# Performance work log

Measured on AMD Instinct MI355X. Metric: run time of the kernel, lower is better.

Reference implementation:

```python
import jax, jax.numpy as jnp
import numpy as np

NOPE, ROPE, LORA, VDIM = 128, 64, 512, 128
H, T = 16, 2048
SCALE = 1.0 / float(np.sqrt(NOPE + ROPE))  # 192**-0.5


def setup_inputs() -> dict:
    key = jax.random.key(0)
    k1, k2, k3, k4, k5 = jax.random.split(key, 5)
    return {
        "query": jax.random.normal(k1, (T, H, NOPE + ROPE), jnp.float32),
        "k_c_normed": jax.random.normal(k2, (T, LORA), jnp.float32),
        "k_pe": jax.random.normal(k3, (T, ROPE), jnp.float32),
        "w_kv_b": jax.random.normal(k4, (LORA, H * (NOPE + VDIM)), jnp.float32) * 0.02,
        "w_uv": jax.random.normal(k5, (H, LORA, VDIM), jnp.float32) * 0.02,
    }


def reference(query, k_c_normed, k_pe, w_kv_b, w_uv):
    # Causal (fresh-token, "compute friendly") MLA path of HPUUnifiedMLAImpl.
    t = query.shape[0]
    # kv_b_proj: latent -> per-head [nope | v]; only k_nope is used for scoring
    kv_nope = (k_c_normed @ w_kv_b).reshape(t, H, NOPE + VDIM)
    k_nope = kv_nope[..., :NOPE]                                   # [T,H,128]
    # k = cat(k_nope, broadcast k_pe) -> [T,H,192]
    k = jnp.concatenate(
        [k_nope, jnp.broadcast_to(k_pe[:, None, :], (t, H, ROPE))], axis=-1)
    # causal attention scores [H,T,T]
    scores = jnp.einsum('thd,shd->hts', query, k) * SCALE
    mask = jnp.tril(jnp.ones((t, t), dtype=bool))                  # causal
    scores = jnp.where(mask[None], scores, jnp.finfo(scores.dtype).min)
    p = jax.nn.softmax(scores, axis=-1)
    # value is the latent k_c, shared across heads (v_causal_latent expand)
    out_latent = jnp.einsum('hts,sl->thl', p, k_c_normed)          # [T,H,512]
    # W_UV projects latent attn output -> full v dim
    out = jnp.einsum('thl,hlv->thv', out_latent, w_uv)             # [T,H,128]
    return out.reshape(t, H * VDIM)
```

## Files before the change

### kernel.cpp

```cpp
#include <hip/hip_runtime.h>
#include <hip/hip_bf16.h>
#include <math.h>

#define T_SEQ 2048
#define NHEAD 16
#define DQK 192
#define DNOPE 128
#define DROPE 64
#define LORA_D 512
#define VDIM 128
#define SCALE_F 0.072168783648703216f
#define KC 32

typedef short bf16x8 __attribute__((ext_vector_type(8)));
typedef float f32x4 __attribute__((ext_vector_type(4)));

static __device__ __forceinline__ unsigned short f2bf(float x) {
  union { float f; unsigned int u; } v; v.f = x;
  unsigned int r = (v.u + 0x7fff + ((v.u >> 16) & 1)) >> 16;
  return (unsigned short)r;
}

__global__ __launch_bounds__(256) void stage_all(
    const float* __restrict__ k_c, const float* __restrict__ w_kv_b,
    const float* __restrict__ w_uv, unsigned short* __restrict__ Ab,
    unsigned short* __restrict__ BkT, unsigned short* __restrict__ BvT)
{
  __shared__ float tile[32][33];
  const int bx = blockIdx.x, role = blockIdx.y;
  const int tid = threadIdx.x;
  if (role == 0) {
    int i = (bx * 256 + tid) * 4;
    float4 v = *(const float4*)(k_c + i);
    ushort4 o = {f2bf(v.x), f2bf(v.y), f2bf(v.z), f2bf(v.w)};
    *(ushort4*)(Ab + i) = o;
    return;
  }
  const int tk = tid >> 3, tc4 = (tid & 7) * 4;
  const int wr = tid >> 3, wk4 = (tid & 7) * 4;
  if (role == 1) {
    const int k0 = (bx & 15) * 32, n0 = (bx >> 4) * 32;
    int n = n0 + tc4;
    int col = n + ((n >> 7) << 7);
    float4 v = *(const float4*)&w_kv_b[(size_t)(k0 + tk) * 4096 + col];
    tile[tk][tc4 + 0] = v.x; tile[tk][tc4 + 1] = v.y;
    tile[tk][tc4 + 2] = v.z; tile[tk][tc4 + 3] = v.w;
    __syncthreads();
    ushort4 o = {f2bf(tile[wk4 + 0][wr]), f2bf(tile[wk4 + 1][wr]),
                 f2bf(tile[wk4 + 2][wr]), f2bf(tile[wk4 + 3][wr])};
    *(ushort4*)&BkT[(size_t)(n0 + wr) * LORA_D + k0 + wk4] = o;
  } else {
    const int k0 = (bx & 15) * 32, v0 = ((bx >> 4) & 3) * 32, h = bx >> 6;
    float4 v = *(const float4*)&w_uv[(size_t)h * 65536 + (size_t)(k0 + tk) * 128 + v0 + tc4];
    tile[tk][tc4 + 0] = v.x; tile[tk][tc4 + 1] = v.y;
    tile[tk][tc4 + 2] = v.z; tile[tk][tc4 + 3] = v.w;
    __syncthreads();
    ushort4 o = {f2bf(tile[wk4 + 0][wr]), f2bf(tile[wk4 + 1][wr]),
                 f2bf(tile[wk4 + 2][wr]), f2bf(tile[wk4 + 3][wr])};
    *(ushort4*)&BvT[(size_t)(h * VDIM + v0 + wr) * LORA_D + k0 + wk4] = o;
  }
}

__global__ __launch_bounds__(256) void prep_gemm(
    const unsigned short* __restrict__ A, const unsigned short* __restrict__ BkT,
    const unsigned short* __restrict__ BvT, const float* __restrict__ k_pe,
    unsigned short* __restrict__ Kb, unsigned short* __restrict__ Vt)
{
  __shared__ unsigned short SMEM[32768];
  const int m0 = blockIdx.x * 128;
  const int by = blockIdx.y;
  const int isK = (by < 16);
  const int n0 = (isK ? by : (by - 16)) * 128;
  const unsigned short* BT = isK ? BkT : BvT;
  const int tid = threadIdx.x;
  const int wid = tid >> 6, lane = tid & 63;
  const int l16 = lane & 15, quad = lane >> 4;
  const int wm = (wid >> 1) * 64, wn = (wid & 1) * 64;

  auto stage_pg = [&](int b, int k0) {
    const char* Asrc = (const char*)(A + (size_t)m0 * LORA_D + k0);
    const char* Bsrc = (const char*)(BT + (size_t)n0 * LORA_D + k0);
    char* Adst = (char*)SMEM + b * 16384;
    char* Bdst = (char*)SMEM + 32768 + b * 16384;
#pragma unroll
    for (int i = 0; i < 4; ++i) {
      int d = tid * 16 + i * 4096;
      int row = d >> 7, c = d & 127;
      int sc = c ^ ((row & 7) << 4);
      __builtin_amdgcn_global_load_lds(
          (const unsigned int*)(Asrc + (size_t)row * 1024 + sc),
          (unsigned int*)(Adst + d), 16, 0, 0);
      __builtin_amdgcn_global_load_lds(
          (const unsigned int*)(Bsrc + (size_t)row * 1024 + sc),
          (unsigned int*)(Bdst + d), 16, 0, 0);
    }
  };

  f32x4 acc[4][4];
#pragma unroll
  for (int i = 0; i < 4; ++i)
#pragma unroll
    for (int j = 0; j < 4; ++j) acc[i][j] = (f32x4){0.f, 0.f, 0.f, 0.f};

  stage_pg(0, 0);
  __syncthreads();
  for (int kc = 0; kc < 8; ++kc) {
    const int cur = kc & 1;
    if (kc < 7) stage_pg(cur ^ 1, (kc + 1) * 64);
#pragma unroll
    for (int kk = 0; kk < 2; ++kk) {
      bf16x8 af[4], bfr[4];
#pragma unroll
      for (int t = 0; t < 4; ++t) {
        int ra = wm + t * 16 + l16;
        af[t] = *(const bf16x8*)((char*)SMEM + cur * 16384 + ra * 128 +
                                 (((kk * 4 + quad) ^ (ra & 7)) << 4));
        int rb = wn + t * 16 + l16;
        bfr[t] = *(const bf16x8*)((char*)SMEM + 32768 + cur * 16384 + rb * 128 +
                                  (((kk * 4 + quad) ^ (rb & 7)) << 4));
      }
#pragma unroll
      for (int mt = 0; mt < 4; ++mt)
#pragma unroll
        for (int nt = 0; nt < 4; ++nt)
          acc[mt][nt] = __builtin_amdgcn_mfma_f32_16x16x32_bf16(af[mt], bfr[nt], acc[mt][nt], 0, 0, 0);
    }
    __syncthreads();
  }

  unsigned short* E = SMEM;
  if (isK) {
#pragma unroll
    for (int mt = 0; mt < 4; ++mt)
#pragma unroll
      for (int nt = 0; nt < 4; ++nt) {
        int ml = wm + mt * 16 + quad * 4;
        int d = wn + nt * 16 + l16;
#pragma unroll
        for (int r = 0; r < 4; ++r)
          E[(ml + r) * 136 + d] = f2bf(acc[mt][nt][r]);
      }
  } else {
#pragma unroll
    for (int mt = 0; mt < 4; ++mt)
#pragma unroll
      for (int nt = 0; nt < 4; ++nt) {
        int ml = wm + mt * 16 + quad * 4;
        int nl = wn + nt * 16 + l16;
#pragma unroll
        for (int r = 0; r < 4; ++r)
          E[nl * 136 + ml + r] = f2bf(acc[mt][nt][r]);
      }
  }
  __syncthreads();

  if (isK) {
    const int h = by;
#pragma unroll
    for (int i = 0; i < 8; ++i) {
      int idx = (i * 256 + tid) * 8;
      int row = idx >> 7, col = idx & 127;
      uint4 v = *(const uint4*)&E[row * 136 + col];
      *(uint4*)&Kb[(size_t)h * (T_SEQ * DQK) + (size_t)(m0 + row) * DQK + col] = v;
    }
    for (int e = tid; e < 128 * 16; e += 256) {
      int row = e >> 4, c4 = (e & 15) * 4;
      float4 v = *(const float4*)&k_pe[(size_t)(m0 + row) * DROPE + c4];
      ushort4 o = {f2bf(v.x), f2bf(v.y), f2bf(v.z), f2bf(v.w)};
      *(ushort4*)&Kb[(size_t)h * (T_SEQ * DQK) + (size_t)(m0 + row) * DQK + DNOPE + c4] = o;
    }
  } else {
#pragma unroll
    for (int i = 0; i < 8; ++i) {
      int idx = (i * 256 + tid) * 8;
      int row = idx >> 7, col = idx & 127;
      uint4 v = *(const uint4*)&E[row * 136 + col];
      *(uint4*)&Vt[(size_t)(n0 + row) * T_SEQ + m0 + col] = v;
    }
  }
}

__global__ __launch_bounds__(256, 3) void flash_mfma(
    const float* __restrict__ Q, const unsigned short* __restrict__ K,
    const unsigned short* __restrict__ Vt, float* __restrict__ outp,
    float* __restrict__ Opart, float* __restrict__ Lpart, int adaptive)
{
  __shared__ unsigned short SM[2 * KC * DQK];
  __shared__ unsigned short Vsm[2 * VDIM * KC];
  __shared__ unsigned short Ps[4][16][40];
  const int id = blockIdx.x;
  const int h = ((id & 7) << 1) | ((id >> 3) & 1);
  int q0, c0, c1, slot, direct;
  if (adaptive) {
    const int b = 79 - (id >> 4);
    int j, sp, s;
    if (b < 8)       { j = b;               sp = 0;            s = 1; }
    else if (b < 24) { j = 8 + (b - 8) / 2; sp = (b - 8) % 2;  s = 2; }
    else if (b < 48) { j = 16 + (b - 24) / 3; sp = (b - 24) % 3; s = 3; }
    else             { j = 24 + (b - 48) / 4; sp = (b - 48) % 4; s = 4; }
    q0 = j * 64;
    const int n = 2 * j + 2;
    c0 = (n * sp) / s;
    c1 = (n * (sp + 1)) / s;
    direct = (s == 1);
    slot = h * 72 + (b - 8);
  } else {
    q0 = (31 - (id >> 4)) * 64;
    c0 = 0; c1 = q0 / KC + 2; direct = 1; slot = 0;
  }
  const int tid = threadIdx.x;
  const int wid = tid >> 6;
  const int lane = tid & 63;
  const int l16 = lane & 15;
  const int quad = lane >> 4;
  const int myrow = q0 + wid * 16 + quad * 4;
  const int nch = c1 - c0;

  const unsigned short* Kh = K + (size_t)h * T_SEQ * DQK;
  const unsigned short* Vth = Vt + (size_t)h * VDIM * T_SEQ;

  int ksrc_off[3], kdst_off[3];
#pragma unroll
  for (int i = 0; i < 3; ++i) {
    int d = tid * 16 + i * 4096;
    int rho = d / 384, c = d - rho * 384;
    int g = ((rho & 15) << 1) | (rho >> 4);
    ksrc_off[i] = g * 384 + (c ^ ((rho & 7) << 4));
    kdst_off[i] = d;
  }
  size_t vsrc_off[2]; int vdst_off[2];
#pragma unroll
  for (int i = 0; i < 2; ++i) {
    int d = tid * 16 + i * 4096;
    int row = d >> 6, c = d & 63;
    vsrc_off[i] = (size_t)row * (T_SEQ * 2) + (c ^ ((row & 3) << 4));
    vdst_off[i] = d;
  }

  auto stage = [&](int buf, int s0) {
    const char* Kc = (const char*)Kh + (size_t)s0 * 384;
    char* Kd = (char*)&SM[buf * (KC * DQK)];
#pragma unroll
    for (int i = 0; i < 3; ++i)
      __builtin_amdgcn_global_load_lds(
          (const unsigned int*)(Kc + ksrc_off[i]),
          (unsigned int*)(Kd + kdst_off[i]), 16, 0, 0);
    const char* Vc = (const char*)Vth + (size_t)s0 * 2;
    char* Vd = (char*)&Vsm[buf * (VDIM * KC)];
#pragma unroll
    for (int i = 0; i < 2; ++i)
      __builtin_amdgcn_global_load_lds(
          (const unsigned int*)(Vc + vsrc_off[i]),
          (unsigned int*)(Vd + vdst_off[i]), 16, 0, 0);
  };

  for (int e = tid; e < 64 * 48; e += 256) {
    int row = e / 48, col = (e % 48) * 4;
    float4 q4 = *(const float4*)&Q[(size_t)(q0 + row) * (NHEAD * DQK) + h * DQK + col];
    ushort4 qp = {f2bf(q4.x), f2bf(q4.y), f2bf(q4.z), f2bf(q4.w)};
    *(ushort4*)&SM[row * DQK + col] = qp;
  }
  __syncthreads();
  bf16x8 qf[6];
#pragma unroll
  for (int ks = 0; ks < 6; ++ks)
    qf[ks] = *(const bf16x8*)&SM[(wid * 16 + l16) * DQK + ks * 32 + quad * 8];
  __syncthreads();
  stage(0, c0 * KC);
  __syncthreads();

  f32x4 oacc[8];
#pragma unroll
  for (int i = 0; i < 8; ++i) oacc[i] = (f32x4){0.f, 0.f, 0.f, 0.f};
  float lsum[4] = {0.f, 0.f, 0.f, 0.f};
  const int kv2 = 2 * l16;

  for (int ck = 0; ck < nch; ++ck) {
    const int cur = ck & 1;
    const int s0 = (c0 + ck) * KC;
    if (ck + 1 < nch) stage(cur ^ 1, s0 + KC);

    const char* Kbase = (const char*)&SM[cur * (KC * DQK)];
    f32x4 sacc[2];
    sacc[0] = (f32x4){0.f, 0.f, 0.f, 0.f};
    sacc[1] = (f32x4){0.f, 0.f, 0.f, 0.f};
    __builtin_amdgcn_s_setprio(1);
#pragma unroll
    for (int ks = 0; ks < 6; ++ks) {
      int c = ks * 64 + quad * 16;
      int r0 = l16, r1 = 16 + l16;
      bf16x8 kf0 = *(const bf16x8*)(Kbase + r0 * 384 + (c ^ ((r0 & 7) << 4)));
      bf16x8 kf1 = *(const bf16x8*)(Kbase + r1 * 384 + (c ^ ((r1 & 7) << 4)));
      sacc[0] = __builtin_amdgcn_mfma_f32_16x16x32_bf16(qf[ks], kf0, sacc[0], 0, 0, 0);
      sacc[1] = __builtin_amdgcn_mfma_f32_16x16x32_bf16(qf[ks], kf1, sacc[1], 0, 0, 0);
    }
    __builtin_amdgcn_s_setprio(0);

    const int kvg = s0 + kv2;
#pragma unroll
    for (int r = 0; r < 4; ++r) {
      int row = myrow + r;
      float p0 = (kvg <= row)     ? __expf(sacc[0][r] * SCALE_F) : 0.f;
      float p1 = (kvg + 1 <= row) ? __expf(sacc[1][r] * SCALE_F) : 0.f;
      lsum[r] += p0 + p1;
      unsigned int pk;
      asm("v_cvt_pk_bf16_f32 %0, %1, %2" : "=v"(pk) : "v"(p0), "v"(p1));
      *(unsigned int*)&Ps[wid][quad * 4 + r][kv2] = pk;
    }

    bf16x8 pf = *(const bf16x8*)&Ps[wid][l16][quad * 8];
    const char* Vbase = (const char*)&Vsm[cur * (VDIM * KC)];
    __builtin_amdgcn_s_setprio(1);
#pragma unroll
    for (int nt = 0; nt < 8; ++nt) {
      int vrow = nt * 16 + l16;
      bf16x8 vf = *(const bf16x8*)(Vbase + vrow * 64 + ((quad * 16) ^ ((vrow & 3) << 4)));
      oacc[nt] = __builtin_amdgcn_mfma_f32_16x16x32_bf16(pf, vf, oacc[nt], 0, 0, 0);
    }
    __builtin_amdgcn_s_setprio(0);

    __syncthreads();
  }

#pragma unroll
  for (int off = 1; off < 16; off <<= 1)
#pragma unroll
    for (int r = 0; r < 4; ++r) lsum[r] += __shfl_xor(lsum[r], off);

  if (direct) {
    float inv[4];
#pragma unroll
    for (int r = 0; r < 4; ++r) inv[r] = 1.f / lsum[r];
#pragma unroll
    for (int nt = 0; nt < 8; ++nt)
#pragma unroll
      for (int r = 0; r < 4; ++r)
        outp[(size_t)(myrow + r) * (NHEAD * VDIM) + h * VDIM + nt * 16 + l16] =
            oacc[nt][r] * inv[r];
  } else {
    const int rbase = wid * 16 + quad * 4;
#pragma unroll
    for (int nt = 0; nt < 8; ++nt)
#pragma unroll
      for (int r = 0; r < 4; ++r)
        Opart[(size_t)slot * 8192 + (rbase + r) * 128 + nt * 16 + l16] =
            oacc[nt][r];
    if (l16 == 0)
#pragma unroll
      for (int r = 0; r < 4; ++r)
        Lpart[slot * 64 + rbase + r] = lsum[r];
  }
}

__global__ __launch_bounds__(256) void reduce_out(
    const float* __restrict__ Opart, const float* __restrict__ Lpart,
    float* __restrict__ outp)
{
  const int t = blockIdx.x;
  const int h = t & 15;
  const int j = 8 + (t >> 4);
  int s, b0;
  if (j < 16)      { s = 2; b0 = 8 + (j - 8) * 2; }
  else if (j < 24) { s = 3; b0 = 24 + (j - 16) * 3; }
  else             { s = 4; b0 = 48 + (j - 24) * 4; }
  const int slot = h * 72 + (b0 - 8);
  const int q0 = j * 64;
  const int tid = threadIdx.x;
#pragma unroll
  for (int i = 0; i < 8; ++i) {
    const int f4 = tid + i * 256;
    const int row = f4 >> 5, cc = f4 & 31;
    float ax = 0.f, ay = 0.f, az = 0.f, aw = 0.f, l = 0.f;
    for (int k = 0; k < s; ++k) {
      float4 v = ((const float4*)Opart)[(size_t)(slot + k) * 2048 + f4];
      ax += v.x; ay += v.y; az += v.z; aw += v.w;
      l += Lpart[(slot + k) * 64 + row];
    }
    const float inv = 1.f / l;
    float4 o = {ax * inv, ay * inv, az * inv, aw * inv};
    ((float4*)outp)[(size_t)(q0 + row) * 512 + h * 32 + cc] = o;
  }
}

extern "C" void kernel_launch(void* const* d_in, const int* in_sizes, int n_in,
                              void* d_out, int out_size, void* d_ws, size_t ws_size,
                              hipStream_t stream) {
  const float* query  = (const float*)d_in[0];
  const float* k_c    = (const float*)d_in[1];
  const float* k_pe   = (const float*)d_in[2];
  const float* w_kv_b = (const float*)d_in[3];
  const float* w_uv   = (const float*)d_in[4];
  float* outp = (float*)d_out;

  unsigned short* Kb  = (unsigned short*)d_ws;
  unsigned short* Vt  = Kb + (size_t)NHEAD * T_SEQ * DQK;
  unsigned short* Ab  = Vt + (size_t)NHEAD * VDIM * T_SEQ;
  unsigned short* BkT = Ab + (size_t)T_SEQ * LORA_D;
  unsigned short* BvT = BkT + (size_t)2048 * LORA_D;
  float* Opart = (float*)(BvT + (size_t)2048 * LORA_D);
  float* Lpart = Opart + (size_t)16 * 72 * 64 * 128;
  const size_t need =
      (size_t)((char*)(Lpart + (size_t)16 * 72 * 64) - (char*)d_ws);
  const int adaptive = (ws_size >= need) ? 1 : 0;

  stage_all<<<dim3(1024, 3), 256, 0, stream>>>(k_c, w_kv_b, w_uv, Ab, BkT, BvT);
  prep_gemm<<<dim3(16, 32), 256, 0, stream>>>(Ab, BkT, BvT, k_pe, Kb, Vt);
  flash_mfma<<<adaptive ? 1280 : 512, 256, 0, stream>>>(query, Kb, Vt, outp,
                                                        Opart, Lpart, adaptive);
  if (adaptive)
    reduce_out<<<384, 256, 0, stream>>>(Opart, Lpart, outp);
}
```

Before: 168.9 us.

## Compute transposed scores and build P fragment via shuffles, dropping LDS staging

Swaps the MFMA operand order so the score tile comes out transposed (query rows along lanes). The probability fragment for the PV MFMA is then assembled in registers with cross-lane shuffles instead of being written to and read back from an LDS scratch buffer. Removing that buffer lets the launch bounds be raised to 4 blocks per CU, and the K row permutation in staging is dropped since it is no longer needed. The row-sum reduction is reorganised to match. This trades LDS traffic for more shuffle instructions and adds register pressure under the tighter occupancy bound.

```diff
diff --git a/kernel.cpp b/kernel.cpp
--- a/kernel.cpp
+++ b/kernel.cpp
@@ -180,14 +180,13 @@
   }
 }
 
-__global__ __launch_bounds__(256, 3) void flash_mfma(
+__global__ __launch_bounds__(256, 4) void flash_mfma(
     const float* __restrict__ Q, const unsigned short* __restrict__ K,
     const unsigned short* __restrict__ Vt, float* __restrict__ outp,
     float* __restrict__ Opart, float* __restrict__ Lpart, int adaptive)
 {
   __shared__ unsigned short SM[2 * KC * DQK];
   __shared__ unsigned short Vsm[2 * VDIM * KC];
-  __shared__ unsigned short Ps[4][16][40];
   const int id = blockIdx.x;
   const int h = ((id & 7) << 1) | ((id >> 3) & 1);
   int q0, c0, c1, slot, direct;
@@ -214,6 +213,7 @@
   const int l16 = lane & 15;
   const int quad = lane >> 4;
   const int myrow = q0 + wid * 16 + quad * 4;
+  const int qrow  = q0 + wid * 16 + l16;
   const int nch = c1 - c0;
 
   const unsigned short* Kh = K + (size_t)h * T_SEQ * DQK;
@@ -224,8 +224,7 @@
   for (int i = 0; i < 3; ++i) {
     int d = tid * 16 + i * 4096;
     int rho = d / 384, c = d - rho * 384;
-    int g = ((rho & 15) << 1) | (rho >> 4);
-    ksrc_off[i] = g * 384 + (c ^ ((rho & 7) << 4));
+    ksrc_off[i] = rho * 384 + (c ^ ((rho & 7) << 4));
     kdst_off[i] = d;
   }
   size_t vsrc_off[2]; int vdst_off[2];
@@ -272,8 +271,7 @@
   f32x4 oacc[8];
 #pragma unroll
   for (int i = 0; i < 8; ++i) oacc[i] = (f32x4){0.f, 0.f, 0.f, 0.f};
-  float lsum[4] = {0.f, 0.f, 0.f, 0.f};
-  const int kv2 = 2 * l16;
+  float lsum = 0.f;
 
   for (int ck = 0; ck < nch; ++ck) {
     const int cur = ck & 1;
@@ -281,9 +279,8 @@
     if (ck + 1 < nch) stage(cur ^ 1, s0 + KC);
 
     const char* Kbase = (const char*)&SM[cur * (KC * DQK)];
-    f32x4 sacc[2];
-    sacc[0] = (f32x4){0.f, 0.f, 0.f, 0.f};
-    sacc[1] = (f32x4){0.f, 0.f, 0.f, 0.f};
+    f32x4 sacc0 = (f32x4){0.f, 0.f, 0.f, 0.f};
+    f32x4 sacc1 = (f32x4){0.f, 0.f, 0.f, 0.f};
     __builtin_amdgcn_s_setprio(1);
 #pragma unroll
     for (int ks = 0; ks < 6; ++ks) {
@@ -291,24 +288,39 @@
       int r0 = l16, r1 = 16 + l16;
       bf16x8 kf0 = *(const bf16x8*)(Kbase + r0 * 384 + (c ^ ((r0 & 7) << 4)));
       bf16x8 kf1 = *(const bf16x8*)(Kbase + r1 * 384 + (c ^ ((r1 & 7) << 4)));
-      sacc[0] = __builtin_amdgcn_mfma_f32_16x16x32_bf16(qf[ks], kf0, sacc[0], 0, 0, 0);
-      sacc[1] = __builtin_amdgcn_mfma_f32_16x16x32_bf16(qf[ks], kf1, sacc[1], 0, 0, 0);
+      sacc0 = __builtin_amdgcn_mfma_f32_16x16x32_bf16(kf0, qf[ks], sacc0, 0, 0, 0);
+      sacc1 = __builtin_amdgcn_mfma_f32_16x16x32_bf16(kf1, qf[ks], sacc1, 0, 0, 0);
     }
     __builtin_amdgcn_s_setprio(0);
 
-    const int kvg = s0 + kv2;
+    float p0[4], p1[4];
 #pragma unroll
     for (int r = 0; r < 4; ++r) {
-      int row = myrow + r;
-      float p0 = (kvg <= row)     ? __expf(sacc[0][r] * SCALE_F) : 0.f;
-      float p1 = (kvg + 1 <= row) ? __expf(sacc[1][r] * SCALE_F) : 0.f;
-      lsum[r] += p0 + p1;
-      unsigned int pk;
-      asm("v_cvt_pk_bf16_f32 %0, %1, %2" : "=v"(pk) : "v"(p0), "v"(p1));
-      *(unsigned int*)&Ps[wid][quad * 4 + r][kv2] = pk;
-    }
-
-    bf16x8 pf = *(const bf16x8*)&Ps[wid][l16][quad * 8];
+      int kva = s0 + quad * 4 + r;
+      p0[r] = (kva <= qrow)      ? __expf(sacc0[r] * SCALE_F) : 0.f;
+      p1[r] = (kva + 16 <= qrow) ? __expf(sacc1[r] * SCALE_F) : 0.f;
+      lsum += p0[r] + p1[r];
+    }
+    unsigned int A0, A1, B0, B1;
+    asm("v_cvt_pk_bf16_f32 %0, %1, %2" : "=v"(A0) : "v"(p0[0]), "v"(p0[1]));
+    asm("v_cvt_pk_bf16_f32 %0, %1, %2" : "=v"(A1) : "v"(p0[2]), "v"(p0[3]));
+    asm("v_cvt_pk_bf16_f32 %0, %1, %2" : "=v"(B0) : "v"(p1[0]), "v"(p1[1]));
+    asm("v_cvt_pk_bf16_f32 %0, %1, %2" : "=v"(B1) : "v"(p1[2]), "v"(p1[3]));
+
+    const int srcA = l16 + ((quad & 1) << 5);
+    const int srcB = srcA + 16;
+    int xa0 = __shfl((int)A0, srcA, 64), ya0 = __shfl((int)B0, srcA, 64);
+    int xa1 = __shfl((int)A1, srcA, 64), ya1 = __shfl((int)B1, srcA, 64);
+    int xb0 = __shfl((int)A0, srcB, 64), yb0 = __shfl((int)B0, srcB, 64);
+    int xb1 = __shfl((int)A1, srcB, 64), yb1 = __shfl((int)B1, srcB, 64);
+    const bool lower = (quad < 2);
+    union { unsigned int u[4]; bf16x8 v; } pw;
+    pw.u[0] = lower ? (unsigned)xa0 : (unsigned)ya0;
+    pw.u[1] = lower ? (unsigned)xa1 : (unsigned)ya1;
+    pw.u[2] = lower ? (unsigned)xb0 : (unsigned)yb0;
+    pw.u[3] = lower ? (unsigned)xb1 : (unsigned)yb1;
+    bf16x8 pf = pw.v;
+
     const char* Vbase = (const char*)&Vsm[cur * (VDIM * KC)];
     __builtin_amdgcn_s_setprio(1);
 #pragma unroll
@@ -322,15 +334,16 @@
     __syncthreads();
   }
 
-#pragma unroll
-  for (int off = 1; off < 16; off <<= 1)
-#pragma unroll
-    for (int r = 0; r < 4; ++r) lsum[r] += __shfl_xor(lsum[r], off);
+  lsum += __shfl_xor(lsum, 16);
+  lsum += __shfl_xor(lsum, 32);
+  float rowsum[4];
+#pragma unroll
+  for (int r = 0; r < 4; ++r) rowsum[r] = __shfl(lsum, quad * 4 + r, 64);
 
   if (direct) {
     float inv[4];
 #pragma unroll
-    for (int r = 0; r < 4; ++r) inv[r] = 1.f / lsum[r];
+    for (int r = 0; r < 4; ++r) inv[r] = 1.f / rowsum[r];
 #pragma unroll
     for (int nt = 0; nt < 8; ++nt)
 #pragma unroll
@@ -348,7 +361,7 @@
     if (l16 == 0)
 #pragma unroll
       for (int r = 0; r < 4; ++r)
-        Lpart[slot * 64 + rbase + r] = lsum[r];
+        Lpart[slot * 64 + rbase + r] = rowsum[r];
   }
 }
 
```

After: 166.4 us. No clear change (-1.5%).
